# Kernel optimization log

Measured on AMD Instinct MI355X. Metric: run time of the kernel, lower is better.

Reference implementation:

```python
import jax, jax.numpy as jnp
import numpy as np

B, S, D, H = 4, 2048, 512, 8
DEPTH = D // H
BAND = 16  # log_thresholds [1,2,4,8,16] union == distance <= 16


def setup_inputs() -> dict:
    key = jax.random.key(0)
    ks = jax.random.split(key, 11)
    sc = 0.02
    return {
        "q": jax.random.normal(ks[0], (B, S, D), jnp.float32),
        "k": jax.random.normal(ks[1], (B, S, D), jnp.float32),
        "v": jax.random.normal(ks[2], (B, S, D), jnp.float32),
        "wq": jax.random.normal(ks[3], (D, D), jnp.float32) * sc,
        "bq": jnp.zeros((D,), jnp.float32),
        "wk": jax.random.normal(ks[4], (D, D), jnp.float32) * sc,
        "bk": jnp.zeros((D,), jnp.float32),
        "wv": jax.random.normal(ks[5], (D, D), jnp.float32) * sc,
        "bv": jnp.zeros((D,), jnp.float32),
        "wo": jax.random.normal(ks[6], (D, D), jnp.float32) * sc,
        "bo": jnp.zeros((D,), jnp.float32),
    }


def _split_heads(x):
    # [B,S,D] -> [B,H,S,depth]
    b, s, _ = x.shape
    return x.reshape(b, s, H, DEPTH).transpose(0, 2, 1, 3)


def reference(q, k, v, wq, bq, wk, bk, wv, bv, wo, bo):
    qh = _split_heads(q @ wq + bq)
    kh = _split_heads(k @ wk + bk)
    vh = _split_heads(v @ wv + bv)
    scale = 1.0 / jnp.sqrt(jnp.float32(DEPTH))
    logits = jnp.einsum("bhqd,bhkd->bhqk", qh, kh) * scale  # [B,H,S,S]
    idx = jnp.arange(S)
    keep = jnp.abs(idx[:, None] - idx[None, :]) <= BAND  # band mask [S,S]
    logits = jnp.where(keep[None, None], logits, jnp.float32(-1e9))
    attn = jax.nn.softmax(logits, axis=-1)
    out = jnp.einsum("bhqk,bhkd->bhqd", attn, vh)
    out = out.transpose(0, 2, 1, 3).reshape(q.shape[0], -1, D)
    return out @ wo + bo
```

## Files before the change

### kernel.cpp

```cpp
#include <hip/hip_runtime.h>

typedef unsigned int uint;
typedef unsigned short ushort;
typedef __attribute__((ext_vector_type(8))) short bf16x8;
typedef __attribute__((ext_vector_type(4))) float f32x4;

namespace {
constexpr int kS = 2048;
constexpr int kD = 512;
constexpr int kH = 8;
constexpr int kNT = 8192;
constexpr int kBand = 16;
}

static __device__ __forceinline__ ushort f2bf(float f) {
  uint u = __builtin_bit_cast(uint, f);
  u = (u + 0x7fffu + ((u >> 16) & 1u)) >> 16;
  return (ushort)u;
}

#define GLD16(gp, lp)                                                   \
  __builtin_amdgcn_global_load_lds(                                     \
      (const __attribute__((address_space(1))) uint*)(gp),              \
      (__attribute__((address_space(3))) uint*)(lp), 16, 0, 0)

__global__ __launch_bounds__(256) void prep_kernel(
    const float* __restrict__ q, const float* __restrict__ k,
    const float* __restrict__ v, const float* __restrict__ wq,
    const float* __restrict__ wk, const float* __restrict__ wv,
    const float* __restrict__ wo, ushort* __restrict__ qb,
    ushort* __restrict__ kb, ushort* __restrict__ vb,
    ushort* __restrict__ WT) {
  __shared__ float Ws[64][65];
  const int blk = blockIdx.x;
  const int tid = threadIdx.x;
  if (blk < 6144) {
    const int z = blk >> 11, t = blk & 2047;
    const float* src = z == 0 ? q : (z == 1 ? k : v);
    ushort* dst = z == 0 ? qb : (z == 1 ? kb : vb);
    const size_t i8 = ((size_t)t * 256 + tid) * 8;
    const float4 x0 = *(const float4*)(src + i8);
    const float4 x1 = *(const float4*)(src + i8 + 4);
    alignas(16) ushort t8[8] = {f2bf(x0.x), f2bf(x0.y), f2bf(x0.z), f2bf(x0.w),
                                f2bf(x1.x), f2bf(x1.y), f2bf(x1.z), f2bf(x1.w)};
    *(uint4*)(dst + i8) = *(const uint4*)t8;
    return;
  }
  const int w = blk - 6144;
  const int z = w >> 6;
  const float* W = z == 0 ? wq : (z == 1 ? wk : (z == 2 ? wv : wo));
  ushort* T = WT + (size_t)z * kD * kD;
  const int kt = ((w >> 3) & 7) * 64, nt = (w & 7) * 64;
  const int r = tid >> 2, c0 = (tid & 3) * 16;
#pragma unroll
  for (int i = 0; i < 4; ++i) {
    const float4 x =
        *(const float4*)(W + (size_t)(kt + r) * kD + nt + c0 + i * 4);
    Ws[r][c0 + i * 4 + 0] = x.x;
    Ws[r][c0 + i * 4 + 1] = x.y;
    Ws[r][c0 + i * 4 + 2] = x.z;
    Ws[r][c0 + i * 4 + 3] = x.w;
  }
  __syncthreads();
  const int n = tid >> 2, k0 = (tid & 3) * 16;
  alignas(16) ushort tmp[16];
#pragma unroll
  for (int i = 0; i < 16; ++i) tmp[i] = f2bf(Ws[k0 + i][n]);
  ushort* dst = T + (size_t)(nt + n) * kD + kt + k0;
  *(uint4*)(dst + 0) = *(const uint4*)&tmp[0];
  *(uint4*)(dst + 8) = *(const uint4*)&tmp[8];
}

template <int TM>
__global__ __launch_bounds__(256) void gemm_kernel(
    const ushort* __restrict__ qb, const ushort* __restrict__ kb,
    const ushort* __restrict__ vb, const ushort* __restrict__ obp,
    const ushort* __restrict__ WT, const float* __restrict__ bq,
    const float* __restrict__ bk, const float* __restrict__ bv,
    const float* __restrict__ bo, ushort* __restrict__ Qp,
    ushort* __restrict__ Kp, ushort* __restrict__ VT,
    float* __restrict__ outp, int mode_arg) {
  const int mode = mode_arg + blockIdx.z;
  const ushort* Ab;
  const float* bias;
  switch (mode) {
    case 0: Ab = qb; bias = bq; break;
    case 1: Ab = kb; bias = bk; break;
    case 2: Ab = vb; bias = bv; break;
    default: Ab = obp; bias = bo; break;
  }
  const ushort* BT = WT + (size_t)mode * kD * kD;

  constexpr int A_STAGE = TM * 32;
  constexpr int B_BASE = 3 * A_STAGE;
  constexpr int NI = (TM == 128) ? 4 : 2;
  constexpr int AI = TM / 64;
  __shared__ alignas(16) ushort smem[B_BASE + 12288];

  const int tid = threadIdx.x;
  const int wave = tid >> 6, lane = tid & 63, l15 = lane & 15, qd = lane >> 4;
  const int wm = (TM == 128) ? (wave >> 1) * 64 : 0;
  const int wn = (TM == 128) ? (wave & 1) * 64 : wave * 32;
  const int lin = blockIdx.x;
  const int xcd = lin & 7, j = lin >> 3;
  const int rblk = xcd + 8 * (j >> 2), cblk = j & 3;
  const int row0 = rblk * TM, col0 = cblk * 128;
  const int sw = (l15 & 3) ^ (l15 >> 2);

  const ushort* pA[AI];
  const ushort* pB[2];
  uint ldsA[AI], ldsB[2];
#pragma unroll
  for (int i = 0; i < AI; ++i) {
    const int linear = i * 256 + tid;
    const int r = linear >> 2, c = linear & 3;
    const int g = c ^ ((r & 3) ^ ((r >> 2) & 3));
    pA[i] = Ab + (size_t)(row0 + r) * kD + g * 8;
    ldsA[i] = (uint)(i * 256 + wave * 64) * 8;
  }
#pragma unroll
  for (int i = 0; i < 2; ++i) {
    const int linear = i * 256 + tid;
    const int r = linear >> 2, c = linear & 3;
    const int g = c ^ ((r & 3) ^ ((r >> 2) & 3));
    pB[i] = BT + (size_t)(col0 + r) * kD + g * 8;
    ldsB[i] = (uint)B_BASE + (uint)(i * 256 + wave * 64) * 8;
  }

#define ISSUE(kk, st)                                                     \
  {                                                                       \
    _Pragma("unroll") for (int i = 0; i < AI; ++i)                        \
        GLD16(pA[i] + (kk), &smem[ldsA[i] + (st) * A_STAGE]);             \
    _Pragma("unroll") for (int i = 0; i < 2; ++i)                         \
        GLD16(pB[i] + (kk), &smem[ldsB[i] + (st) * 4096]);                \
  }

  f32x4 acc[4][NI];
#pragma unroll
  for (int mi = 0; mi < 4; ++mi)
#pragma unroll
    for (int ni = 0; ni < NI; ++ni) acc[mi][ni] = (f32x4)(0.f);

  ISSUE(0, 0);
  ISSUE(32, 1);
#pragma unroll
  for (int it = 0; it < 16; ++it) {
    if (it < 15) {
      if constexpr (TM == 128)
        asm volatile("s_waitcnt vmcnt(4) lgkmcnt(0)\n\ts_barrier" ::: "memory");
      else
        asm volatile("s_waitcnt vmcnt(3) lgkmcnt(0)\n\ts_barrier" ::: "memory");
    } else {
      asm volatile("s_waitcnt vmcnt(0) lgkmcnt(0)\n\ts_barrier" ::: "memory");
    }
    if (it < 14) ISSUE((it + 2) * 32, (it + 2) % 3);
    const ushort* as = &smem[(it % 3) * A_STAGE];
    const ushort* bs = &smem[B_BASE + (it % 3) * 4096];
    bf16x8 af[4], br[NI];
#pragma unroll
    for (int mi = 0; mi < 4; ++mi)
      af[mi] = *(const bf16x8*)&as[(wm + mi * 16 + l15) * 32 + (qd ^ sw) * 8];
#pragma unroll
    for (int ni = 0; ni < NI; ++ni)
      br[ni] = *(const bf16x8*)&bs[(wn + ni * 16 + l15) * 32 + (qd ^ sw) * 8];
#pragma unroll
    for (int mi = 0; mi < 4; ++mi)
#pragma unroll
      for (int ni = 0; ni < NI; ++ni)
        acc[mi][ni] = __builtin_amdgcn_mfma_f32_16x16x32_bf16(
            af[mi], br[ni], acc[mi][ni], 0, 0, 0);
  }
#undef ISSUE

  float bcol[NI];
#pragma unroll
  for (int ni = 0; ni < NI; ++ni) bcol[ni] = bias[col0 + wn + ni * 16 + l15];

  if (mode == 3) {
#pragma unroll
    for (int mi = 0; mi < 4; ++mi)
#pragma unroll
      for (int ni = 0; ni < NI; ++ni) {
        const int n_g = col0 + wn + ni * 16 + l15;
#pragma unroll
        for (int r = 0; r < 4; ++r) {
          const int token = row0 + wm + mi * 16 + qd * 4 + r;
          outp[(size_t)token * kD + n_g] = acc[mi][ni][r] + bcol[ni];
        }
      }
    return;
  }

  __syncthreads();

  ushort* T = &smem[wave * 4608];
  if (mode <= 1) {
#pragma unroll
    for (int mi = 0; mi < 4; ++mi)
#pragma unroll
      for (int ni = 0; ni < NI; ++ni)
#pragma unroll
        for (int r = 0; r < 4; ++r)
          T[(mi * 16 + qd * 4 + r) * 72 + ni * 16 + l15] =
              f2bf(acc[mi][ni][r] + bcol[ni]);
  } else {
#pragma unroll
    for (int mi = 0; mi < 4; ++mi)
#pragma unroll
      for (int ni = 0; ni < NI; ++ni)
#pragma unroll
        for (int r = 0; r < 4; ++r)
          T[(ni * 16 + l15) * 72 + mi * 16 + qd * 4 + r] =
              f2bf(acc[mi][ni][r] + bcol[ni]);
  }
  asm volatile("s_waitcnt lgkmcnt(0)" ::: "memory");

  const ushort* Trow = &smem[wave * 4608 + lane * 72];
  if (mode <= 1) {
    ushort* C = (mode == 0) ? Qp : Kp;
    ushort* dst = C + (size_t)(row0 + wm + lane) * kD + col0 + wn;
#pragma unroll
    for (int c = 0; c < 8; ++c)
      *(uint4*)(dst + c * 8) = *(const uint4*)(Trow + c * 8);
  } else {
    const int n_g = col0 + wn + lane;
    const int h = n_g >> 6, d = n_g & 63;
    const int t0 = row0 + wm;
    const int b = t0 >> 11, ss = t0 & (kS - 1);
    ushort* dst = VT + ((size_t)(b * kH + h) * 64 + d) * kS + ss;
#pragma unroll
    for (int c = 0; c < 8; ++c)
      *(uint4*)(dst + c * 8) = *(const uint4*)(Trow + c * 8);
  }
}

__global__ __launch_bounds__(64, 1) void attn_kernel(
    const ushort* __restrict__ Qp, const ushort* __restrict__ Kp,
    const ushort* __restrict__ VT, ushort* __restrict__ Ob) {
  __shared__ alignas(16) ushort Pl[64 * 104];

  const int lane = threadIdx.x, l15 = lane & 15, qd = lane >> 4;
  const int bh = blockIdx.y, b = bh >> 3, h = bh & 7;
  const int q0 = blockIdx.x * 64;
  const int colA = h * 64;

  bf16x8 qf[4][2], kf[6][2];
#pragma unroll
  for (int mi = 0; mi < 4; ++mi) {
    const size_t base =
        ((size_t)b * kS + q0 + mi * 16 + l15) * kD + colA + qd * 8;
#pragma unroll
    for (int kc = 0; kc < 2; ++kc)
      qf[mi][kc] = *(const bf16x8*)&Qp[base + kc * 32];
  }
#pragma unroll
  for (int ni = 0; ni < 6; ++ni) {
    int key = q0 - kBand + ni * 16 + l15;
    key = key < 0 ? 0 : (key > kS - 1 ? kS - 1 : key);
    const size_t base = ((size_t)b * kS + key) * kD + colA + qd * 8;
#pragma unroll
    for (int kc = 0; kc < 2; ++kc)
      kf[ni][kc] = *(const bf16x8*)&Kp[base + kc * 32];
  }

  f32x4 S[4][6];
#pragma unroll
  for (int mi = 0; mi < 4; ++mi)
#pragma unroll
    for (int ni = 0; ni < 6; ++ni) S[mi][ni] = (f32x4)(0.f);
#pragma unroll
  for (int mi = 0; mi < 4; ++mi)
#pragma unroll
    for (int ni = 0; ni < 6; ++ni)
#pragma unroll
      for (int kc = 0; kc < 2; ++kc)
        S[mi][ni] = __builtin_amdgcn_mfma_f32_16x16x32_bf16(
            qf[mi][kc], kf[ni][kc], S[mi][ni], 0, 0, 0);

#pragma unroll
  for (int mi = 0; mi < 4; ++mi)
#pragma unroll
    for (int ni = 0; ni < 6; ++ni)
#pragma unroll
      for (int r = 0; r < 4; ++r) {
        const int q_local = mi * 16 + qd * 4 + r;
        const int key_local = ni * 16 + l15;
        const int key = q0 - kBand + key_local;
        const int dlt = key_local - q_local;
        const bool ok = (dlt >= 0) && (dlt <= 32) && (key >= 0) && (key < kS);
        S[mi][ni][r] = ok ? S[mi][ni][r] * 0.125f : -3.0e38f;
      }

  float inv[4][4];
#pragma unroll
  for (int mi = 0; mi < 4; ++mi)
#pragma unroll
    for (int r = 0; r < 4; ++r) {
      float m = S[mi][0][r];
#pragma unroll
      for (int ni = 1; ni < 6; ++ni) m = fmaxf(m, S[mi][ni][r]);
      m = fmaxf(m, __shfl_xor(m, 1));
      m = fmaxf(m, __shfl_xor(m, 2));
      m = fmaxf(m, __shfl_xor(m, 4));
      m = fmaxf(m, __shfl_xor(m, 8));
      float s = 0.f;
#pragma unroll
      for (int ni = 0; ni < 6; ++ni) {
        const float e = __expf(S[mi][ni][r] - m);
        S[mi][ni][r] = e;
        s += e;
      }
      s += __shfl_xor(s, 1);
      s += __shfl_xor(s, 2);
      s += __shfl_xor(s, 4);
      s += __shfl_xor(s, 8);
      inv[mi][r] = 1.f / s;
    }

#pragma unroll
  for (int mi = 0; mi < 4; ++mi)
#pragma unroll
    for (int ni = 0; ni < 6; ++ni)
#pragma unroll
      for (int r = 0; r < 4; ++r)
        Pl[(mi * 16 + qd * 4 + r) * 104 + ni * 16 + l15] = f2bf(S[mi][ni][r]);
  __syncthreads();

  f32x4 O[4][4];
#pragma unroll
  for (int mi = 0; mi < 4; ++mi)
#pragma unroll
    for (int nt = 0; nt < 4; ++nt) O[mi][nt] = (f32x4)(0.f);

#pragma unroll
  for (int kc = 0; kc < 3; ++kc) {
    bf16x8 pf[4], vfr[4];
#pragma unroll
    for (int mi = 0; mi < 4; ++mi)
      pf[mi] = *(const bf16x8*)&Pl[(mi * 16 + l15) * 104 + kc * 32 + qd * 8];
    int kb0 = q0 - kBand + kc * 32 + qd * 8;
    kb0 = kb0 < 0 ? 0 : (kb0 > kS - 8 ? kS - 8 : kb0);
#pragma unroll
    for (int nt = 0; nt < 4; ++nt)
      vfr[nt] =
          *(const bf16x8*)&VT[((size_t)bh * 64 + nt * 16 + l15) * kS + kb0];
#pragma unroll
    for (int mi = 0; mi < 4; ++mi)
#pragma unroll
      for (int nt = 0; nt < 4; ++nt)
        O[mi][nt] = __builtin_amdgcn_mfma_f32_16x16x32_bf16(pf[mi], vfr[nt],
                                                            O[mi][nt], 0, 0, 0);
  }

#pragma unroll
  for (int mi = 0; mi < 4; ++mi)
#pragma unroll
    for (int nt = 0; nt < 4; ++nt)
#pragma unroll
      for (int r = 0; r < 4; ++r)
        Pl[(mi * 16 + qd * 4 + r) * 72 + nt * 16 + l15] =
            f2bf(O[mi][nt][r] * inv[mi][r]);
  asm volatile("s_waitcnt lgkmcnt(0)" ::: "memory");

  ushort* dst = Ob + ((size_t)b * kS + q0 + lane) * kD + colA;
  const ushort* Trow = &Pl[lane * 72];
#pragma unroll
  for (int c = 0; c < 8; ++c)
    *(uint4*)(dst + c * 8) = *(const uint4*)(Trow + c * 8);
}

extern "C" void kernel_launch(void* const* d_in, const int* in_sizes, int n_in,
                              void* d_out, int out_size, void* d_ws,
                              size_t ws_size, hipStream_t stream) {
  const float* q = (const float*)d_in[0];
  const float* k = (const float*)d_in[1];
  const float* v = (const float*)d_in[2];
  const float* wq = (const float*)d_in[3];
  const float* bq = (const float*)d_in[4];
  const float* wk = (const float*)d_in[5];
  const float* bk = (const float*)d_in[6];
  const float* wv = (const float*)d_in[7];
  const float* bv = (const float*)d_in[8];
  const float* wo = (const float*)d_in[9];
  const float* bo = (const float*)d_in[10];
  float* out = (float*)d_out;

  const size_t n1 = (size_t)kNT * kD;
  ushort* qb = (ushort*)d_ws;
  ushort* kb = qb + n1;
  ushort* vb = kb + n1;
  ushort* Qp = vb + n1;
  ushort* Kp = Qp + n1;
  ushort* VT = Kp + n1;
  ushort* Ob = VT + n1;
  ushort* WT = Ob + n1;

  prep_kernel<<<dim3(6400), 256, 0, stream>>>(q, k, v, wq, wk, wv, wo, qb, kb,
                                              vb, WT);
  gemm_kernel<128><<<dim3(256, 1, 3), 256, 0, stream>>>(
      qb, kb, vb, Ob, WT, bq, bk, bv, bo, Qp, Kp, VT, out, 0);
  attn_kernel<<<dim3(kS / 64, 32), 64, 0, stream>>>(Qp, Kp, VT, Ob);
  gemm_kernel<64><<<dim3(512, 1, 1), 256, 0, stream>>>(
      qb, kb, vb, Ob, WT, bq, bk, bv, bo, Qp, Kp, VT, out, 3);
}
```

Baseline: 157.7 us.

## Fuse fp32-to-bf16 input conversion into the QKV projection GEMM A-loader

Removes the separate pass that converts q/k/v from fp32 to bf16 in the workspace. The QKV GEMM now loads fp32 A tiles into registers, converts them and writes them swizzled into LDS, double-buffering in registers alongside the existing async B loads. This avoids writing and re-reading three bf16 activation copies. In exchange the A path no longer uses direct global-to-LDS DMA, which adds VGPR pressure and LDS write instructions inside the main loop.

Result: slower. 165.2 us (+4.7%).

```diff
diff --git a/kernel.cpp b/kernel.cpp
--- a/kernel.cpp
+++ b/kernel.cpp
@@ -24,29 +24,13 @@
       (const __attribute__((address_space(1))) uint*)(gp),              \
       (__attribute__((address_space(3))) uint*)(lp), 16, 0, 0)
 
-__global__ __launch_bounds__(256) void prep_kernel(
-    const float* __restrict__ q, const float* __restrict__ k,
-    const float* __restrict__ v, const float* __restrict__ wq,
-    const float* __restrict__ wk, const float* __restrict__ wv,
-    const float* __restrict__ wo, ushort* __restrict__ qb,
-    ushort* __restrict__ kb, ushort* __restrict__ vb,
+__global__ __launch_bounds__(256) void prep_w_kernel(
+    const float* __restrict__ wq, const float* __restrict__ wk,
+    const float* __restrict__ wv, const float* __restrict__ wo,
     ushort* __restrict__ WT) {
   __shared__ float Ws[64][65];
-  const int blk = blockIdx.x;
+  const int w = blockIdx.x;
   const int tid = threadIdx.x;
-  if (blk < 6144) {
-    const int z = blk >> 11, t = blk & 2047;
-    const float* src = z == 0 ? q : (z == 1 ? k : v);
-    ushort* dst = z == 0 ? qb : (z == 1 ? kb : vb);
-    const size_t i8 = ((size_t)t * 256 + tid) * 8;
-    const float4 x0 = *(const float4*)(src + i8);
-    const float4 x1 = *(const float4*)(src + i8 + 4);
-    alignas(16) ushort t8[8] = {f2bf(x0.x), f2bf(x0.y), f2bf(x0.z), f2bf(x0.w),
-                                f2bf(x1.x), f2bf(x1.y), f2bf(x1.z), f2bf(x1.w)};
-    *(uint4*)(dst + i8) = *(const uint4*)t8;
-    return;
-  }
-  const int w = blk - 6144;
   const int z = w >> 6;
   const float* W = z == 0 ? wq : (z == 1 ? wk : (z == 2 ? wv : wo));
   ushort* T = WT + (size_t)z * kD * kD;
@@ -71,22 +55,23 @@
   *(uint4*)(dst + 8) = *(const uint4*)&tmp[8];
 }
 
-template <int TM>
+template <int TM, bool F32A>
 __global__ __launch_bounds__(256) void gemm_kernel(
-    const ushort* __restrict__ qb, const ushort* __restrict__ kb,
-    const ushort* __restrict__ vb, const ushort* __restrict__ obp,
+    const float* __restrict__ qf, const float* __restrict__ kf,
+    const float* __restrict__ vf, const ushort* __restrict__ obp,
     const ushort* __restrict__ WT, const float* __restrict__ bq,
     const float* __restrict__ bk, const float* __restrict__ bv,
     const float* __restrict__ bo, ushort* __restrict__ Qp,
     ushort* __restrict__ Kp, ushort* __restrict__ VT,
     float* __restrict__ outp, int mode_arg) {
   const int mode = mode_arg + blockIdx.z;
-  const ushort* Ab;
+  const float* Af = nullptr;
+  const ushort* Ab = nullptr;
   const float* bias;
   switch (mode) {
-    case 0: Ab = qb; bias = bq; break;
-    case 1: Ab = kb; bias = bk; break;
-    case 2: Ab = vb; bias = bv; break;
+    case 0: Af = qf; bias = bq; break;
+    case 1: Af = kf; bias = bk; break;
+    case 2: Af = vf; bias = bv; break;
     default: Ab = obp; bias = bo; break;
   }
   const ushort* BT = WT + (size_t)mode * kD * kD;
@@ -107,17 +92,8 @@
   const int row0 = rblk * TM, col0 = cblk * 128;
   const int sw = (l15 & 3) ^ (l15 >> 2);
 
-  const ushort* pA[AI];
   const ushort* pB[2];
-  uint ldsA[AI], ldsB[2];
-#pragma unroll
-  for (int i = 0; i < AI; ++i) {
-    const int linear = i * 256 + tid;
-    const int r = linear >> 2, c = linear & 3;
-    const int g = c ^ ((r & 3) ^ ((r >> 2) & 3));
-    pA[i] = Ab + (size_t)(row0 + r) * kD + g * 8;
-    ldsA[i] = (uint)(i * 256 + wave * 64) * 8;
-  }
+  uint ldsB[2];
 #pragma unroll
   for (int i = 0; i < 2; ++i) {
     const int linear = i * 256 + tid;
@@ -126,13 +102,50 @@
     pB[i] = BT + (size_t)(col0 + r) * kD + g * 8;
     ldsB[i] = (uint)B_BASE + (uint)(i * 256 + wave * 64) * 8;
   }
-
-#define ISSUE(kk, st)                                                     \
-  {                                                                       \
-    _Pragma("unroll") for (int i = 0; i < AI; ++i)                        \
-        GLD16(pA[i] + (kk), &smem[ldsA[i] + (st) * A_STAGE]);             \
-    _Pragma("unroll") for (int i = 0; i < 2; ++i)                         \
-        GLD16(pB[i] + (kk), &smem[ldsB[i] + (st) * 4096]);                \
+#define ISSUE_B(kk, st)                                \
+  {                                                    \
+    GLD16(pB[0] + (kk), &smem[ldsB[0] + (st) * 4096]); \
+    GLD16(pB[1] + (kk), &smem[ldsB[1] + (st) * 4096]); \
+  }
+
+  const ushort* pA[AI];
+  uint ldsAd[AI];
+  const float* pAf[4];
+  uint ldsAw[4];
+  float4 afp[2][4];
+  if constexpr (!F32A) {
+#pragma unroll
+    for (int i = 0; i < AI; ++i) {
+      const int linear = i * 256 + tid;
+      const int r = linear >> 2, c = linear & 3;
+      const int g = c ^ ((r & 3) ^ ((r >> 2) & 3));
+      pA[i] = Ab + (size_t)(row0 + r) * kD + g * 8;
+      ldsAd[i] = (uint)(i * 256 + wave * 64) * 8;
+    }
+  } else {
+#pragma unroll
+    for (int i = 0; i < 4; ++i) {
+      const int idx = i * 256 + tid;
+      const int r = idx >> 3, c = idx & 7;
+      pAf[i] = Af + (size_t)(row0 + r) * kD + c * 4;
+      ldsAw[i] =
+          (uint)(r * 32 + (((c >> 1) ^ ((r & 3) ^ ((r >> 2) & 3))) * 8) +
+                 (c & 1) * 4);
+    }
+  }
+#define ISSUE_A_DMA(kk, st)                                   \
+  {                                                           \
+    _Pragma("unroll") for (int i = 0; i < AI; ++i)            \
+        GLD16(pA[i] + (kk), &smem[ldsAd[i] + (st) * A_STAGE]); \
+  }
+#define CVT_WRITE_A(st, buf)                                            \
+  {                                                                     \
+    _Pragma("unroll") for (int i = 0; i < 4; ++i) {                     \
+      const float4 x = afp[buf][i];                                     \
+      const uint lo = (uint)f2bf(x.x) | ((uint)f2bf(x.y) << 16);        \
+      const uint hi = (uint)f2bf(x.z) | ((uint)f2bf(x.w) << 16);        \
+      *(uint2*)&smem[ldsAw[i] + (st) * A_STAGE] = make_uint2(lo, hi);   \
+    }                                                                   \
   }
 
   f32x4 acc[4][NI];
@@ -141,19 +154,47 @@
 #pragma unroll
     for (int ni = 0; ni < NI; ++ni) acc[mi][ni] = (f32x4)(0.f);
 
-  ISSUE(0, 0);
-  ISSUE(32, 1);
+  if constexpr (F32A) {
+#pragma unroll
+    for (int i = 0; i < 4; ++i) afp[0][i] = *(const float4*)(pAf[i] + 0);
+    ISSUE_B(0, 0);
+    ISSUE_B(32, 1);
+#pragma unroll
+    for (int i = 0; i < 4; ++i) afp[1][i] = *(const float4*)(pAf[i] + 32);
+    CVT_WRITE_A(0, 0);
+  } else {
+    ISSUE_A_DMA(0, 0);
+    ISSUE_B(0, 0);
+    ISSUE_A_DMA(32, 1);
+    ISSUE_B(32, 1);
+  }
+
 #pragma unroll
   for (int it = 0; it < 16; ++it) {
     if (it < 15) {
-      if constexpr (TM == 128)
+      if constexpr (F32A)
+        asm volatile("s_waitcnt vmcnt(6) lgkmcnt(0)\n\ts_barrier" ::: "memory");
+      else if constexpr (TM == 128)
         asm volatile("s_waitcnt vmcnt(4) lgkmcnt(0)\n\ts_barrier" ::: "memory");
       else
         asm volatile("s_waitcnt vmcnt(3) lgkmcnt(0)\n\ts_barrier" ::: "memory");
     } else {
       asm volatile("s_waitcnt vmcnt(0) lgkmcnt(0)\n\ts_barrier" ::: "memory");
     }
-    if (it < 14) ISSUE((it + 2) * 32, (it + 2) % 3);
+    if constexpr (F32A) {
+      if (it < 14) ISSUE_B((it + 2) * 32, (it + 2) % 3);
+      if (it < 15) CVT_WRITE_A((it + 1) % 3, (it + 1) & 1);
+      if (it < 14) {
+#pragma unroll
+        for (int i = 0; i < 4; ++i)
+          afp[it & 1][i] = *(const float4*)(pAf[i] + (it + 2) * 32);
+      }
+    } else {
+      if (it < 14) {
+        ISSUE_A_DMA((it + 2) * 32, (it + 2) % 3);
+        ISSUE_B((it + 2) * 32, (it + 2) % 3);
+      }
+    }
     const ushort* as = &smem[(it % 3) * A_STAGE];
     const ushort* bs = &smem[B_BASE + (it % 3) * 4096];
     bf16x8 af[4], br[NI];
@@ -170,7 +211,9 @@
         acc[mi][ni] = __builtin_amdgcn_mfma_f32_16x16x32_bf16(
             af[mi], br[ni], acc[mi][ni], 0, 0, 0);
   }
-#undef ISSUE
+#undef ISSUE_B
+#undef ISSUE_A_DMA
+#undef CVT_WRITE_A
 
   float bcol[NI];
 #pragma unroll
@@ -386,20 +429,16 @@
   float* out = (float*)d_out;
 
   const size_t n1 = (size_t)kNT * kD;
-  ushort* qb = (ushort*)d_ws;
-  ushort* kb = qb + n1;
-  ushort* vb = kb + n1;
-  ushort* Qp = vb + n1;
+  ushort* Qp = (ushort*)d_ws;
   ushort* Kp = Qp + n1;
   ushort* VT = Kp + n1;
   ushort* Ob = VT + n1;
   ushort* WT = Ob + n1;
 
-  prep_kernel<<<dim3(6400), 256, 0, stream>>>(q, k, v, wq, wk, wv, wo, qb, kb,
-                                              vb, WT);
-  gemm_kernel<128><<<dim3(256, 1, 3), 256, 0, stream>>>(
-      qb, kb, vb, Ob, WT, bq, bk, bv, bo, Qp, Kp, VT, out, 0);
+  prep_w_kernel<<<dim3(256), 256, 0, stream>>>(wq, wk, wv, wo, WT);
+  gemm_kernel<128, true><<<dim3(256, 1, 3), 256, 0, stream>>>(
+      q, k, v, Ob, WT, bq, bk, bv, bo, Qp, Kp, VT, out, 0);
   attn_kernel<<<dim3(kS / 64, 32), 64, 0, stream>>>(Qp, Kp, VT, Ob);
-  gemm_kernel<64><<<dim3(512, 1, 1), 256, 0, stream>>>(
-      qb, kb, vb, Ob, WT, bq, bk, bv, bo, Qp, Kp, VT, out, 3);
-}
+  gemm_kernel<64, false><<<dim3(512, 1, 1), 256, 0, stream>>>(
+      q, k, v, Ob, WT, bq, bk, bv, bo, Qp, Kp, VT, out, 3);
+}
```
